# Optimization experiments

Measured on AMD Instinct MI355X. Metric: run time of the kernel, lower is better.

## Reference

```python
import jax, jax.numpy as jnp
import numpy as np

RES = 512       # grid resolution per plane
NFEAT = 32      # features per plane level
LRELU_SLOPE = 0.2
PLANE_AXES = ((0, 1), (0, 2), (1, 2))  # NPlaneSum: xy, xz, yz planes


def encode_nplanesum(x_t, planes):
    """x_t: [N,3] in [0,1]; planes: [3,RES,RES,NFEAT]. Bilinear interp on 3 planes, summed."""
    pos = x_t * (RES - 1)                      # [N,3]
    p0f = jnp.floor(pos)
    frac = pos - p0f                           # [N,3]
    p0 = jnp.clip(p0f.astype(jnp.int32), 0, RES - 1)
    p1 = jnp.minimum(p0 + 1, RES - 1)
    h = jnp.zeros((x_t.shape[0], NFEAT), dtype=planes.dtype)
    for k, (a, b) in enumerate(PLANE_AXES):
        pl = planes[k]                         # [RES,RES,NFEAT]
        i0, i1 = p0[:, a], p1[:, a]
        j0, j1 = p0[:, b], p1[:, b]
        fa = frac[:, a:a + 1]
        fb = frac[:, b:b + 1]
        v00 = pl[i0, j0]; v01 = pl[i0, j1]
        v10 = pl[i1, j0]; v11 = pl[i1, j1]
        h = h + (v00 * (1 - fb) + v01 * fb) * (1 - fa) + (v10 * (1 - fb) + v11 * fb) * fa
    return h


def decode_fp16(h, W1, b1, W2, b2):
    """Tiny MLP run in fp16 (as in Decoder), equal_lr scaling = 1/sqrt(fan_in)."""
    s = np.float16(1.0 / np.sqrt(NFEAT))
    y = h.astype(jnp.float16)
    y = jnp.dot(y, W1.astype(jnp.float16) * s) + b1.astype(jnp.float16)
    y = jnp.where(y >= 0, y, jnp.float16(LRELU_SLOPE) * y)   # LeakyReLU(0.2)
    y = jnp.dot(y, W2.astype(jnp.float16) * s) + b2.astype(jnp.float16)
    return y.astype(jnp.float32)                             # [N,4]


def setup_inputs() -> dict:
    key = jax.random.key(0)
    k1, k2, k3, k4 = jax.random.split(key, 4)
    N = 2_097_152
    x = jax.random.uniform(k1, (N, 3), dtype=jnp.float32, minval=-1.0, maxval=1.0)
    planes = jax.random.normal(k2, (3, RES, RES, NFEAT), dtype=jnp.float32) * 0.05
    W1 = jax.random.normal(k3, (NFEAT, NFEAT), dtype=jnp.float32)
    b1 = jnp.zeros((NFEAT,), dtype=jnp.float32)
    W2 = jax.random.normal(k4, (NFEAT, 4), dtype=jnp.float32)
    b2 = jnp.zeros((4,), dtype=jnp.float32)
    return {"x": x, "planes": planes, "W1": W1, "b1": b1, "W2": W2, "b2": b2}


def reference(x, planes, W1, b1, W2, b2):
    # transform_points is identity (K=None); map [-1,1] -> [0,1]
    x_t = (x + 1.0) * 0.5
    h = encode_nplanesum(x_t, planes)
    out = decode_fp16(h, W1, b1, W2, b2)           # [N,4]
    sdf = out[..., 0]
    rgb = (jnp.tanh(out[..., 1:]) + 1.0) * 0.5
    # analytic normals: d(sdf)/d(x_t), matching forward_sdf_nablas
    sdf_sum = lambda xt: decode_fp16(encode_nplanesum(xt, planes), W1, b1, W2, b2)[..., 0].sum()
    nablas = jax.grad(sdf_sum)(x_t)                # [N,3]
    return sdf, h, nablas, rgb
```

## Files before the change

### kernel.cpp

```cpp
#include <hip/hip_runtime.h>
#include <hip/hip_fp16.h>

#define RES 512
#define NF 32

static __device__ __forceinline__ float h2f(float v) {
    return __half2float(__float2half(v));
}

#define GET(v, c) ((c) == 0 ? (v).x : ((c) == 1 ? (v).y : ((c) == 2 ? (v).z : (v).w)))

__global__ __launch_bounds__(256) void stylesdf_fused(
    const float* __restrict__ x,
    const float* __restrict__ planes,
    const float* __restrict__ W1,
    const float* __restrict__ b1,
    const float* __restrict__ W2,
    const float* __restrict__ b2,
    float* __restrict__ out, int N)
{
#pragma clang fp contract(off)
    __shared__ __align__(16) float sW1[NF * NF];
    __shared__ __align__(16) float sW1T[NF * NF];
    __shared__ __align__(16) float sW2[NF * 4];
    __shared__ __align__(16) float sB1[NF];
    __shared__ __align__(16) float sB2[4];
    __shared__ __align__(16) float sW2c0[NF];

    const float S16 = h2f(0.17677669529663687f);
    const float LREL = h2f(0.2f);

    const int tid = threadIdx.x;
    for (int idx = tid; idx < NF * NF; idx += 256) {
        float w = h2f(h2f(W1[idx]) * S16);
        sW1[idx] = w;
        sW1T[(idx & 31) * NF + (idx >> 5)] = w;
    }
    if (tid < NF * 4) sW2[tid] = h2f(h2f(W2[tid]) * S16);
    if (tid < NF) { sB1[tid] = h2f(b1[tid]); sW2c0[tid] = h2f(h2f(W2[tid * 4]) * S16); }
    if (tid < 4) sB2[tid] = h2f(b2[tid]);
    __syncthreads();

    const int gt = blockIdx.x * 256 + tid;
    const int p = gt >> 2;
    if (p >= N) return;
    const int q = gt & 3;
    const int f0 = q << 3;
    const int lane4 = (tid & 63) << 2;
    const int base4 = lane4 & ~15;

    float fr0, fr1, fr2;
    int a0lo, a0hi, a1lo, a1hi, a2lo, a2hi;
#define AXIS(c, FR, LO, HI)                                 \
    {                                                       \
        float xt = (x[3 * p + (c)] + 1.0f) * 0.5f;          \
        float pos = xt * 511.0f;                            \
        float pf = floorf(pos);                             \
        FR = pos - pf;                                      \
        int qq = (int)pf;                                   \
        qq = qq < 0 ? 0 : (qq > 511 ? 511 : qq);            \
        LO = qq;                                            \
        HI = (qq + 1 > 511) ? 511 : qq + 1;                 \
    }
    AXIS(0, fr0, a0lo, a0hi)
    AXIS(1, fr1, a1lo, a1hi)
    AXIS(2, fr2, a2lo, a2hi)
#undef AXIS

    const int oA00 = (a0lo * RES + a1lo) << 5, oA01 = (a0lo * RES + a1hi) << 5;
    const int oA10 = (a0hi * RES + a1lo) << 5, oA11 = (a0hi * RES + a1hi) << 5;
    const int oB00 = (a0lo * RES + a2lo) << 5, oB01 = (a0lo * RES + a2hi) << 5;
    const int oB10 = (a0hi * RES + a2lo) << 5, oB11 = (a0hi * RES + a2hi) << 5;
    const int oC00 = (a1lo * RES + a2lo) << 5, oC01 = (a1lo * RES + a2hi) << 5;
    const int oC10 = (a1hi * RES + a2lo) << 5, oC11 = (a1hi * RES + a2hi) << 5;
    const float* pl0 = planes;
    const float* pl1 = planes + RES * RES * NF;
    const float* pl2 = planes + 2 * (RES * RES * NF);

#define LD4(b, off) (*(const float4*)((b) + (off)))

    const float ifa01 = 1.0f - fr0, ifb01 = 1.0f - fr1;
    const float ifa02 = 1.0f - fr0, ifb02 = 1.0f - fr2;
    const float ifa12 = 1.0f - fr1, ifb12 = 1.0f - fr2;

    float hl[8];
    float d0l[8], d1l[8], d2l[8];
    float4* ho = (float4*)(out + (size_t)N + (size_t)p * NF);

#pragma unroll
    for (int kk = 0; kk < 2; ++kk) {
        const int fo = f0 + 4 * kk;
        const float4 vA00 = LD4(pl0, oA00 + fo), vA01 = LD4(pl0, oA01 + fo);
        const float4 vA10 = LD4(pl0, oA10 + fo), vA11 = LD4(pl0, oA11 + fo);
        const float4 vB00 = LD4(pl1, oB00 + fo), vB01 = LD4(pl1, oB01 + fo);
        const float4 vB10 = LD4(pl1, oB10 + fo), vB11 = LD4(pl1, oB11 + fo);
        const float4 vC00 = LD4(pl2, oC00 + fo), vC01 = LD4(pl2, oC01 + fo);
        const float4 vC10 = LD4(pl2, oC10 + fo), vC11 = LD4(pl2, oC11 + fo);
        float hc[4];
#pragma unroll
        for (int c = 0; c < 4; ++c) {
            const int f = 4 * kk + c;
            {
                const float a00 = GET(vA00, c), a01 = GET(vA01, c);
                const float a10 = GET(vA10, c), a11 = GET(vA11, c);
                const float t4 = (a00 * ifb01 + a01 * fr1) * ifa01;
                const float t8 = (a10 * ifb01 + a11 * fr1) * fr0;
                hc[c] = t4 + t8;
                d0l[f] = (a10 - a00) * ifb01 + (a11 - a01) * fr1;
                d1l[f] = (a01 - a00) * ifa01 + (a11 - a10) * fr0;
            }
            {
                const float a00 = GET(vB00, c), a01 = GET(vB01, c);
                const float a10 = GET(vB10, c), a11 = GET(vB11, c);
                const float t4 = (a00 * ifb02 + a01 * fr2) * ifa02;
                const float t8 = (a10 * ifb02 + a11 * fr2) * fr0;
                hc[c] = (hc[c] + t4) + t8;
                d0l[f] += (a10 - a00) * ifb02 + (a11 - a01) * fr2;
                d2l[f] = (a01 - a00) * ifa02 + (a11 - a10) * fr0;
            }
            {
                const float a00 = GET(vC00, c), a01 = GET(vC01, c);
                const float a10 = GET(vC10, c), a11 = GET(vC11, c);
                const float t4 = (a00 * ifb12 + a01 * fr2) * ifa12;
                const float t8 = (a10 * ifb12 + a11 * fr2) * fr1;
                hc[c] = (hc[c] + t4) + t8;
                d1l[f] += (a10 - a00) * ifb12 + (a11 - a01) * fr2;
                d2l[f] += (a01 - a00) * ifa12 + (a11 - a10) * fr1;
            }
            hl[f] = h2f(hc[c]);
        }
        ho[2 * q + kk] = make_float4(hc[0], hc[1], hc[2], hc[3]);
    }

    float y[8];
#pragma unroll
    for (int jj = 0; jj < 8; ++jj) y[jj] = 0.f;
#pragma unroll
    for (int i = 0; i < 32; ++i) {
        const float hi = __int_as_float(__builtin_amdgcn_ds_bpermute(
            base4 + 4 * (i >> 3), __float_as_int(hl[i & 7])));
        const float4 wA = *(const float4*)(sW1 + i * NF + f0);
        const float4 wB = *(const float4*)(sW1 + i * NF + f0 + 4);
        y[0] = y[0] + hi * wA.x;
        y[1] = y[1] + hi * wA.y;
        y[2] = y[2] + hi * wA.z;
        y[3] = y[3] + hi * wA.w;
        y[4] = y[4] + hi * wB.x;
        y[5] = y[5] + hi * wB.y;
        y[6] = y[6] + hi * wB.z;
        y[7] = y[7] + hi * wB.w;
    }

    float o0 = 0.f, o1 = 0.f, o2 = 0.f, o3 = 0.f;
    float ml[8];
#pragma unroll
    for (int jj = 0; jj < 8; ++jj) {
        const int j = f0 + jj;
        const float yd = h2f(y[jj]);
        const float y16 = h2f(yd + sB1[j]);
        const bool nn = y16 >= 0.0f;
        const float zj = nn ? y16 : h2f(LREL * y16);
        const float4 w2 = ((const float4*)sW2)[j];
        o0 = o0 + zj * w2.x;
        o1 = o1 + zj * w2.y;
        o2 = o2 + zj * w2.z;
        o3 = o3 + zj * w2.w;
        ml[jj] = (nn ? 1.0f : LREL) * sW2c0[j];
    }

    float gl[8];
#pragma unroll
    for (int ii = 0; ii < 8; ++ii) gl[ii] = 0.f;
#pragma unroll
    for (int j = 0; j < 32; ++j) {
        const float mj = __int_as_float(__builtin_amdgcn_ds_bpermute(
            base4 + 4 * (j >> 3), __float_as_int(ml[j & 7])));
        const float4 wA = *(const float4*)(sW1T + j * NF + f0);
        const float4 wB = *(const float4*)(sW1T + j * NF + f0 + 4);
        gl[0] = fmaf(mj, wA.x, gl[0]);
        gl[1] = fmaf(mj, wA.y, gl[1]);
        gl[2] = fmaf(mj, wA.z, gl[2]);
        gl[3] = fmaf(mj, wA.w, gl[3]);
        gl[4] = fmaf(mj, wB.x, gl[4]);
        gl[5] = fmaf(mj, wB.y, gl[5]);
        gl[6] = fmaf(mj, wB.z, gl[6]);
        gl[7] = fmaf(mj, wB.w, gl[7]);
    }

    float n0 = 0.f, n1 = 0.f, n2 = 0.f;
#pragma unroll
    for (int ii = 0; ii < 8; ++ii) {
        n0 = fmaf(gl[ii], d0l[ii], n0);
        n1 = fmaf(gl[ii], d1l[ii], n1);
        n2 = fmaf(gl[ii], d2l[ii], n2);
    }

#define XADD(v)                                                               \
    v += __int_as_float(__builtin_amdgcn_ds_bpermute(lane4 ^ 4,  __float_as_int(v))); \
    v += __int_as_float(__builtin_amdgcn_ds_bpermute(lane4 ^ 8,  __float_as_int(v)));
    XADD(o0) XADD(o1) XADD(o2) XADD(o3)
    XADD(n0) XADD(n1) XADD(n2)
#undef XADD

    o0 = h2f(h2f(o0) + sB2[0]);
    o1 = h2f(h2f(o1) + sB2[1]);
    o2 = h2f(h2f(o2) + sB2[2]);
    o3 = h2f(h2f(o3) + sB2[3]);
    n0 *= 511.0f; n1 *= 511.0f; n2 *= 511.0f;

    if (q == 0) out[p] = o0;
    if (q == 1) {
        const size_t nb = (size_t)N * 33 + (size_t)p * 3;
        out[nb + 0] = n0; out[nb + 1] = n1; out[nb + 2] = n2;
    }
    if (q == 2) {
        const size_t rb = (size_t)N * 36 + (size_t)p * 3;
        out[rb + 0] = (tanhf(o1) + 1.0f) * 0.5f;
        out[rb + 1] = (tanhf(o2) + 1.0f) * 0.5f;
        out[rb + 2] = (tanhf(o3) + 1.0f) * 0.5f;
    }
#undef LD4
#undef GET
}

extern "C" void kernel_launch(void* const* d_in, const int* in_sizes, int n_in,
                              void* d_out, int out_size, void* d_ws, size_t ws_size,
                              hipStream_t stream) {
    const float* x      = (const float*)d_in[0];
    const float* planes = (const float*)d_in[1];
    const float* W1     = (const float*)d_in[2];
    const float* b1     = (const float*)d_in[3];
    const float* W2     = (const float*)d_in[4];
    const float* b2     = (const float*)d_in[5];
    float* out = (float*)d_out;
    const int N = in_sizes[0] / 3;
    const long long total = 4LL * N;
    const int blocks = (int)((total + 255) / 256);
    stylesdf_fused<<<blocks, 256, 0, stream>>>(x, planes, W1, b1, W2, b2, out, N);
}
```

Before: 893.9 us.

## Use DPP quad broadcasts, interleaved feature mapping and packed fp32 math in MLP

Replaces ds_bpermute cross-lane broadcasts and reductions with DPP quad_perm moves, which avoid the LDS crossbar. Features are remapped so each lane owns features 4q..4q+3 and 16+4q..16+4q+3, which lets each broadcast source come from a fixed quad lane. The MLP forward and gradient dot products are written with 2-wide float vectors so the compiler can emit packed FMA/mul instructions. This changes the gather layout per lane and risks altering rounding order if packed ops fuse differently, but contract is off.

```diff
diff --git a/kernel.cpp b/kernel.cpp
--- a/kernel.cpp
+++ b/kernel.cpp
@@ -4,8 +4,22 @@
 #define RES 512
 #define NF 32
 
+typedef float v2f __attribute__((ext_vector_type(2)));
+
 static __device__ __forceinline__ float h2f(float v) {
     return __half2float(__float2half(v));
+}
+static __device__ __forceinline__ v2f mkv2(float a, float b) { v2f r; r.x = a; r.y = b; return r; }
+
+template <int L>
+static __device__ __forceinline__ float qb(float v) {
+    return __int_as_float(__builtin_amdgcn_mov_dpp(
+        __float_as_int(v), (L | (L << 2) | (L << 4) | (L << 6)), 0xf, 0xf, true));
+}
+static __device__ __forceinline__ float qsum(float v) {
+    v += __int_as_float(__builtin_amdgcn_mov_dpp(__float_as_int(v), 0xB1, 0xf, 0xf, true));
+    v += __int_as_float(__builtin_amdgcn_mov_dpp(__float_as_int(v), 0x4E, 0xf, 0xf, true));
+    return v;
 }
 
 #define GET(v, c) ((c) == 0 ? (v).x : ((c) == 1 ? (v).y : ((c) == 2 ? (v).z : (v).w)))
@@ -45,9 +59,7 @@
     const int p = gt >> 2;
     if (p >= N) return;
     const int q = gt & 3;
-    const int f0 = q << 3;
-    const int lane4 = (tid & 63) << 2;
-    const int base4 = lane4 & ~15;
+    const int fq = q << 2;
 
     float fr0, fr1, fr2;
     int a0lo, a0hi, a1lo, a1hi, a2lo, a2hi;
@@ -89,7 +101,7 @@
 
 #pragma unroll
     for (int kk = 0; kk < 2; ++kk) {
-        const int fo = f0 + 4 * kk;
+        const int fo = fq + 16 * kk;
         const float4 vA00 = LD4(pl0, oA00 + fo), vA01 = LD4(pl0, oA01 + fo);
         const float4 vA10 = LD4(pl0, oA10 + fo), vA11 = LD4(pl0, oA11 + fo);
         const float4 vB00 = LD4(pl1, oB00 + fo), vB01 = LD4(pl1, oB01 + fo);
@@ -129,34 +141,39 @@
             }
             hl[f] = h2f(hc[c]);
         }
-        ho[2 * q + kk] = make_float4(hc[0], hc[1], hc[2], hc[3]);
-    }
-
-    float y[8];
-#pragma unroll
-    for (int jj = 0; jj < 8; ++jj) y[jj] = 0.f;
-#pragma unroll
-    for (int i = 0; i < 32; ++i) {
-        const float hi = __int_as_float(__builtin_amdgcn_ds_bpermute(
-            base4 + 4 * (i >> 3), __float_as_int(hl[i & 7])));
-        const float4 wA = *(const float4*)(sW1 + i * NF + f0);
-        const float4 wB = *(const float4*)(sW1 + i * NF + f0 + 4);
-        y[0] = y[0] + hi * wA.x;
-        y[1] = y[1] + hi * wA.y;
-        y[2] = y[2] + hi * wA.z;
-        y[3] = y[3] + hi * wA.w;
-        y[4] = y[4] + hi * wB.x;
-        y[5] = y[5] + hi * wB.y;
-        y[6] = y[6] + hi * wB.z;
-        y[7] = y[7] + hi * wB.w;
-    }
+        ho[q + 4 * kk] = make_float4(hc[0], hc[1], hc[2], hc[3]);
+    }
+
+    v2f y2[4];
+    y2[0] = mkv2(0.f, 0.f); y2[1] = mkv2(0.f, 0.f);
+    y2[2] = mkv2(0.f, 0.f); y2[3] = mkv2(0.f, 0.f);
+
+#define YSTEP(half, ow, e)                                                     \
+    {                                                                          \
+        const int i = 16 * (half) + 4 * (ow) + (e);                            \
+        const float hi = qb<(ow)>(hl[(e) + 4 * (half)]);                       \
+        const v2f hv = mkv2(hi, hi);                                           \
+        const float4 wA = *(const float4*)(sW1 + i * NF + fq);                 \
+        const float4 wB = *(const float4*)(sW1 + i * NF + fq + 16);            \
+        y2[0] = y2[0] + hv * mkv2(wA.x, wA.y);       \
+        y2[1] = y2[1] + hv * mkv2(wA.z, wA.w);                                 \
+        y2[2] = y2[2] + hv * mkv2(wB.x, wB.y);                                 \
+        y2[3] = y2[3] + hv * mkv2(wB.z, wB.w);                                 \
+    }
+#define Y4(half, ow) YSTEP(half, ow, 0) YSTEP(half, ow, 1) YSTEP(half, ow, 2) YSTEP(half, ow, 3)
+#define Y16(half) Y4(half, 0) Y4(half, 1) Y4(half, 2) Y4(half, 3)
+    Y16(0) Y16(1)
+#undef Y16
+#undef Y4
+#undef YSTEP
 
     float o0 = 0.f, o1 = 0.f, o2 = 0.f, o3 = 0.f;
     float ml[8];
 #pragma unroll
-    for (int jj = 0; jj < 8; ++jj) {
-        const int j = f0 + jj;
-        const float yd = h2f(y[jj]);
+    for (int t = 0; t < 8; ++t) {
+        const int j = fq + (t & 3) + 16 * (t >> 2);
+        const float yt = (t & 1) ? y2[t >> 1].y : y2[t >> 1].x;
+        const float yd = h2f(yt);
         const float y16 = h2f(yd + sB1[j]);
         const bool nn = y16 >= 0.0f;
         const float zj = nn ? y16 : h2f(LREL * y16);
@@ -165,42 +182,43 @@
         o1 = o1 + zj * w2.y;
         o2 = o2 + zj * w2.z;
         o3 = o3 + zj * w2.w;
-        ml[jj] = (nn ? 1.0f : LREL) * sW2c0[j];
-    }
-
-    float gl[8];
-#pragma unroll
-    for (int ii = 0; ii < 8; ++ii) gl[ii] = 0.f;
-#pragma unroll
-    for (int j = 0; j < 32; ++j) {
-        const float mj = __int_as_float(__builtin_amdgcn_ds_bpermute(
-            base4 + 4 * (j >> 3), __float_as_int(ml[j & 7])));
-        const float4 wA = *(const float4*)(sW1T + j * NF + f0);
-        const float4 wB = *(const float4*)(sW1T + j * NF + f0 + 4);
-        gl[0] = fmaf(mj, wA.x, gl[0]);
-        gl[1] = fmaf(mj, wA.y, gl[1]);
-        gl[2] = fmaf(mj, wA.z, gl[2]);
-        gl[3] = fmaf(mj, wA.w, gl[3]);
-        gl[4] = fmaf(mj, wB.x, gl[4]);
-        gl[5] = fmaf(mj, wB.y, gl[5]);
-        gl[6] = fmaf(mj, wB.z, gl[6]);
-        gl[7] = fmaf(mj, wB.w, gl[7]);
-    }
+        ml[t] = (nn ? 1.0f : LREL) * sW2c0[j];
+    }
+
+    v2f g2[4];
+    g2[0] = mkv2(0.f, 0.f); g2[1] = mkv2(0.f, 0.f);
+    g2[2] = mkv2(0.f, 0.f); g2[3] = mkv2(0.f, 0.f);
+
+#define GSTEP(half, ow, e)                                                     \
+    {                                                                          \
+        const int j = 16 * (half) + 4 * (ow) + (e);                            \
+        const float mj = qb<(ow)>(ml[(e) + 4 * (half)]);                       \
+        const v2f mv = mkv2(mj, mj);                                           \
+        const float4 wA = *(const float4*)(sW1T + j * NF + fq);                \
+        const float4 wB = *(const float4*)(sW1T + j * NF + fq + 16);           \
+        g2[0] = __builtin_elementwise_fma(mv, mkv2(wA.x, wA.y), g2[0]);        \
+        g2[1] = __builtin_elementwise_fma(mv, mkv2(wA.z, wA.w), g2[1]);        \
+        g2[2] = __builtin_elementwise_fma(mv, mkv2(wB.x, wB.y), g2[2]);        \
+        g2[3] = __builtin_elementwise_fma(mv, mkv2(wB.z, wB.w), g2[3]);        \
+    }
+#define G4(half, ow) GSTEP(half, ow, 0) GSTEP(half, ow, 1) GSTEP(half, ow, 2) GSTEP(half, ow, 3)
+#define G16(half) G4(half, 0) G4(half, 1) G4(half, 2) G4(half, 3)
+    G16(0) G16(1)
+#undef G16
+#undef G4
+#undef GSTEP
 
     float n0 = 0.f, n1 = 0.f, n2 = 0.f;
 #pragma unroll
-    for (int ii = 0; ii < 8; ++ii) {
-        n0 = fmaf(gl[ii], d0l[ii], n0);
-        n1 = fmaf(gl[ii], d1l[ii], n1);
-        n2 = fmaf(gl[ii], d2l[ii], n2);
-    }
-
-#define XADD(v)                                                               \
-    v += __int_as_float(__builtin_amdgcn_ds_bpermute(lane4 ^ 4,  __float_as_int(v))); \
-    v += __int_as_float(__builtin_amdgcn_ds_bpermute(lane4 ^ 8,  __float_as_int(v)));
-    XADD(o0) XADD(o1) XADD(o2) XADD(o3)
-    XADD(n0) XADD(n1) XADD(n2)
-#undef XADD
+    for (int t = 0; t < 8; ++t) {
+        const float gt_ = (t & 1) ? g2[t >> 1].y : g2[t >> 1].x;
+        n0 = fmaf(gt_, d0l[t], n0);
+        n1 = fmaf(gt_, d1l[t], n1);
+        n2 = fmaf(gt_, d2l[t], n2);
+    }
+
+    o0 = qsum(o0); o1 = qsum(o1); o2 = qsum(o2); o3 = qsum(o3);
+    n0 = qsum(n0); n1 = qsum(n1); n2 = qsum(n2);
 
     o0 = h2f(h2f(o0) + sB2[0]);
     o1 = h2f(h2f(o1) + sB2[1]);
```

After: 918.5 us. 1.03x slower.
